# Kernel tuning notes

Measured on AMD Instinct MI355X. Metric: run time of the kernel, lower is better.

## Reference

```python
import jax, jax.numpy as jnp
import numpy as np

N = 40000          # nodes
E = 640000         # edges (avg in-degree ~16)
D_IN = 128         # in_dim == out_dim
E_DIM = 16         # edge feature dim
N_AGG = 6          # mean max min std dir1-av dir1-dx
N_SC = 3           # identity amplification attenuation
AVG_D_LOG = float(np.log(16.0))  # avg_d['log']
EPS = 1e-8
STD_EPS = 1e-5


def setup_inputs() -> dict:
    key = jax.random.key(0)
    ks = jax.random.split(key, 10)
    h = jax.random.normal(ks[0], (N, D_IN), jnp.float32)
    e = jax.random.normal(ks[1], (E, E_DIM), jnp.float32)
    eig = jax.random.normal(ks[2], (N, 2), jnp.float32)
    snorm_n = jax.random.uniform(ks[3], (N, 1), jnp.float32)
    src = jax.random.randint(ks[4], (E,), 0, N)
    dst = jax.random.randint(ks[5], (E,), 0, N)
    pre_in = 2 * D_IN + E_DIM
    W_pre = jax.random.normal(ks[6], (pre_in, D_IN), jnp.float32) / np.sqrt(pre_in)
    b_pre = jnp.zeros((D_IN,), jnp.float32)
    post_in = (N_AGG * N_SC + 1) * D_IN
    W_post = jax.random.normal(ks[7], (post_in, D_IN), jnp.float32) / np.sqrt(post_in)
    b_post = jnp.zeros((D_IN,), jnp.float32)
    return {"h": h, "e": e, "eig": eig, "snorm_n": snorm_n, "src": src,
            "dst": dst, "W_pre": W_pre, "b_pre": b_pre,
            "W_post": W_post, "b_post": b_post}


def reference(h, e, eig, snorm_n, src, dst, W_pre, b_pre, W_post, b_post):
    # --- pretrans on edges: MLP(cat(h_src, h_dst, ef)) -> [E, D_IN]
    z = jnp.concatenate([h[src], h[dst], e], axis=1)
    m = z @ W_pre + b_pre

    seg = lambda x: jax.ops.segment_sum(x, dst, num_segments=N)
    deg = seg(jnp.ones((E,), m.dtype))          # in-degree per node [N]
    has = deg > 0
    degc = jnp.maximum(deg, 1.0)

    # --- mailbox aggregators (edge-parallel segment reductions over dst)
    s1 = seg(m)
    mean = s1 / degc[:, None]
    var = seg(m * m) / degc[:, None] - mean * mean
    std = jnp.sqrt(jnp.maximum(var, 0.0) + STD_EPS)
    mx = jnp.where(has[:, None], jax.ops.segment_max(m, dst, num_segments=N), 0.0)
    mn = jnp.where(has[:, None], jax.ops.segment_min(m, dst, num_segments=N), 0.0)
    # eigenvector-directional aggregators (eig index 1), normalized per dst
    d = eig[src, 1] - eig[dst, 1]                              # [E]
    denom = seg(jnp.abs(d)) + EPS                              # [N]
    dir_av = seg(m * (jnp.abs(d) / denom[dst])[:, None])
    dir_dx = seg(m * (d / denom[dst])[:, None]) - h            # uses h_in

    agg = jnp.concatenate([mean, mx, mn, std, dir_av, dir_dx], axis=1)
    agg = jnp.where(has[:, None], agg, 0.0)  # DGL leaves zeros for isolated nodes

    # --- degree scalers: identity / amplification / attenuation
    logd = jnp.log(degc + 1.0)
    amp = agg * (logd / AVG_D_LOG)[:, None]
    att = agg * (AVG_D_LOG / logd)[:, None]
    hcat = jnp.concatenate([h, agg, amp, att], axis=1)  # [N, 19*D_IN]

    # --- posttrans MLP + graph norm + relu + residual (dropout p=0, no batchnorm)
    out = hcat @ W_post + b_post
    out = out * snorm_n
    out = jax.nn.relu(out)
    out = h + out
    return out
```

## Files before the change

kernel.cpp:

```cpp
#include <hip/hip_runtime.h>
#include <hip/hip_bf16.h>
#include <math.h>

typedef __attribute__((ext_vector_type(4))) float f32x4;
typedef __attribute__((ext_vector_type(2))) float f32x2;
typedef __attribute__((ext_vector_type(8))) short short8;
typedef unsigned short ushort_t;
typedef unsigned int uint_t;

__device__ __forceinline__ float b2f(unsigned short u) {
    unsigned int v = ((unsigned int)u) << 16;
    return __uint_as_float(v);
}
__device__ __forceinline__ unsigned short f2b(float f) {
    unsigned int x = __float_as_uint(f);
    unsigned int r = (x + 0x7fffu + ((x >> 16) & 1u)) >> 16;
    return (unsigned short)r;
}

__global__ void prep_kernel(const float* __restrict__ W_pre,
                            const float* __restrict__ W_post,
                            const float* __restrict__ h,
                            int* __restrict__ counts,
                            ushort_t* __restrict__ WbT,
                            ushort_t* __restrict__ WcT,
                            ushort_t* __restrict__ X, int Nn) {
    int i = blockIdx.x * 256 + threadIdx.x;
    int n0 = Nn + 1;
    if (i < n0) { counts[i] = 0; return; }
    i -= n0;
    if (i < 256 * 128) {
        int nn = i >> 7, k = i & 127;
        float v = (nn < 128) ? W_pre[k * 128 + nn] : W_pre[(128 + k) * 128 + (nn - 128)];
        WbT[i] = f2b(v);
        return;
    }
    i -= 256 * 128;
    if (i < 384 * 896) {
        int nn = i / 896, k = i % 896;
        float v;
        if (k < 128) {
            v = (nn < 128) ? W_post[k * 128 + nn] : 0.f;
        } else {
            int ka = k - 128;
            if (nn < 128)      v = W_post[(128 + ka) * 128 + nn];
            else if (nn < 256) v = W_post[(896 + ka) * 128 + (nn - 128)];
            else               v = W_post[(1664 + ka) * 128 + (nn - 256)];
        }
        WcT[i] = f2b(v);
        return;
    }
    i -= 384 * 896;
    if (i < Nn * 32) {
        int n = i >> 5, c4 = (i & 31) * 4;
        float4 hv = *(const float4*)&h[(size_t)n * 128 + c4];
        ushort4 o;
        o.x = f2b(hv.x); o.y = f2b(hv.y); o.z = f2b(hv.z); o.w = f2b(hv.w);
        *(ushort4*)&X[(size_t)n * 896 + c4] = o;
    }
}

__global__ void hist_kernel(const int* __restrict__ dst, int* __restrict__ counts, int E) {
    int i = blockIdx.x * 256 + threadIdx.x;
    if (i < E) atomicAdd(&counts[dst[i]], 1);
}

__global__ __launch_bounds__(1024) void scan_kernel(int* __restrict__ counts,
                                                    int* __restrict__ cursors, int Nn) {
    __shared__ int part[1024];
    int t = threadIdx.x;
    int base = t * 40;
    int vals[40];
#pragma unroll
    for (int c = 0; c < 10; ++c) {
        int idx = base + c * 4;
        int4 v4 = (idx + 3 < Nn) ? *(const int4*)&counts[idx]
                  : make_int4(idx < Nn ? counts[idx] : 0,
                              idx + 1 < Nn ? counts[idx + 1] : 0,
                              idx + 2 < Nn ? counts[idx + 2] : 0,
                              idx + 3 < Nn ? counts[idx + 3] : 0);
        vals[c * 4] = v4.x; vals[c * 4 + 1] = v4.y;
        vals[c * 4 + 2] = v4.z; vals[c * 4 + 3] = v4.w;
    }
    int loc[40];
    int s = 0;
#pragma unroll
    for (int i = 0; i < 40; ++i) { loc[i] = s; s += vals[i]; }
    part[t] = s;
    __syncthreads();
    for (int off = 1; off < 1024; off <<= 1) {
        int v = part[t];
        int u = (t >= off) ? part[t - off] : 0;
        __syncthreads();
        part[t] = v + u;
        __syncthreads();
    }
    int pre = (t > 0) ? part[t - 1] : 0;
#pragma unroll
    for (int i = 0; i < 40; ++i) {
        int idx = base + i;
        if (idx < Nn) { int o = pre + loc[i]; counts[idx] = o; cursors[idx] = o; }
    }
    if (t == 1023) counts[Nn] = part[1023];
}

__global__ void scatter_kernel(const int* __restrict__ dst, const int* __restrict__ src,
                               const float* __restrict__ eig, int* __restrict__ cursors,
                               int4* __restrict__ esl, int E) {
    int i = blockIdx.x * 256 + threadIdx.x;
    if (i < E) {
        int v = dst[i];
        int p = atomicAdd(&cursors[v], 1);
        int s = src[i];
        esl[p] = make_int4(s, i, __float_as_int(eig[s * 2 + 1]), 0);
    }
}

template <int OUT_BF16>
__global__ __launch_bounds__(256) void gemm_bt(const ushort_t* __restrict__ A, int lda,
                                               const ushort_t* __restrict__ Bt, int ldb,
                                               void* __restrict__ Cv, int ldc,
                                               int M, int K, int NT) {
    __shared__ ushort_t ldsbuf[2 * 128 * 64];
    const int tid = threadIdx.x, wid = tid >> 6, lane = tid & 63;
    int nwg = gridDim.x;
    int orig = blockIdx.x;
    int q8 = nwg >> 3, r8 = nwg & 7;
    int xcd = orig & 7, local = orig >> 3;
    int wg = (xcd < r8 ? xcd * (q8 + 1) : r8 * (q8 + 1) + (xcd - r8) * q8) + local;
    const int m0 = (wg / NT) * 128, n0 = (wg % NT) * 128;
    f32x4 acc[4][4] = {};
    const int wrow = (wid >> 1) * 64, wcol = (wid & 1) * 64;

    for (int kt = 0; kt < K; kt += 64) {
#pragma unroll
        for (int rnd = 0; rnd < 4; ++rnd) {
            int libase = rnd * 256 + wid * 64;
            {
                int lc = libase + lane;
                int r = lc >> 3, cs = lc & 7;
                int c = cs ^ (r & 7);
                int row = m0 + r; row = row < M ? row : M - 1;
                const ushort_t* g = A + (size_t)row * lda + (kt + c * 8);
                __builtin_amdgcn_global_load_lds(
                    (const __attribute__((address_space(1))) unsigned int*)g,
                    (__attribute__((address_space(3))) unsigned int*)&ldsbuf[(size_t)libase * 8],
                    16, 0, 0);
            }
            {
                int lc = libase + lane;
                int r = lc >> 3, cs = lc & 7;
                int c = cs ^ (r & 7);
                const ushort_t* g = Bt + (size_t)(n0 + r) * ldb + (kt + c * 8);
                __builtin_amdgcn_global_load_lds(
                    (const __attribute__((address_space(1))) unsigned int*)g,
                    (__attribute__((address_space(3))) unsigned int*)&ldsbuf[8192 + (size_t)libase * 8],
                    16, 0, 0);
            }
        }
        __syncthreads();
#pragma unroll
        for (int kk = 0; kk < 2; ++kk) {
            short8 af[4], bfr[4];
#pragma unroll
            for (int f = 0; f < 4; ++f) {
                int r = wrow + f * 16 + (lane & 15);
                int c16 = kk * 4 + (lane >> 4);
                int ch = r * 8 + (c16 ^ (r & 7));
                af[f] = *(const short8*)&ldsbuf[ch * 8];
            }
#pragma unroll
            for (int f = 0; f < 4; ++f) {
                int r = wcol + f * 16 + (lane & 15);
                int c16 = kk * 4 + (lane >> 4);
                int ch = r * 8 + (c16 ^ (r & 7));
                bfr[f] = *(const short8*)&ldsbuf[8192 + ch * 8];
            }
#pragma unroll
            for (int i = 0; i < 4; ++i)
#pragma unroll
                for (int j = 0; j < 4; ++j)
                    acc[i][j] = __builtin_amdgcn_mfma_f32_16x16x32_bf16(af[i], bfr[j], acc[i][j], 0, 0, 0);
        }
        __syncthreads();
    }
#pragma unroll
    for (int i = 0; i < 4; ++i)
#pragma unroll
        for (int j = 0; j < 4; ++j)
#pragma unroll
            for (int q = 0; q < 4; ++q) {
                int row = m0 + wrow + i * 16 + (lane >> 4) * 4 + q;
                int col = n0 + wcol + j * 16 + (lane & 15);
                if (row < M) {
                    if (OUT_BF16) ((ushort_t*)Cv)[(size_t)row * ldc + col] = f2b(acc[i][j][q]);
                    else          ((float*)Cv)[(size_t)row * ldc + col] = acc[i][j][q];
                }
            }
}

#define RLI(v, l) __builtin_amdgcn_readlane((v), (l))
__global__ __launch_bounds__(256) void agg_coop(
    const ushort_t* __restrict__ PQ, ushort_t* __restrict__ X,
    const int4* __restrict__ esl, const int* __restrict__ offs,
    const float* __restrict__ eig, const float* __restrict__ h,
    const float* __restrict__ ef, const float* __restrict__ W_pre,
    const float* __restrict__ b_pre, float* __restrict__ scal, int Nn) {
    int tid = threadIdx.x;
    int wid = tid >> 6, lane = tid & 63;
    int n = blockIdx.x * 4 + wid;
    if (n >= Nn) return;
    int off0 = offs[n], off1 = offs[n + 1];
    int deg = off1 - off0;
    int d0 = lane * 2;

    f32x2 w3r[16];
#pragma unroll
    for (int j = 0; j < 16; ++j)
        w3r[j] = *(const f32x2*)&W_pre[(256 + j) * 128 + d0];

    uint_t qw = *(const uint_t*)&PQ[(size_t)n * 256 + 128 + d0];
    float2 bp = *(const float2*)&b_pre[d0];
    f32x2 qb;
    qb.x = b2f((ushort_t)(qw & 0xffff)) + bp.x;
    qb.y = b2f((ushort_t)(qw >> 16)) + bp.y;
    float eigd = eig[n * 2 + 1];

    f32x2 s = {0.f, 0.f}, ss = {0.f, 0.f}, av = {0.f, 0.f}, dv = {0.f, 0.f};
    f32x2 mx = {-1e30f, -1e30f}, mn = {1e30f, 1e30f};
    float den = 0.f;

    for (int q0 = off0; q0 < off1; q0 += 16) {
        int cnt = off1 - q0; if (cnt > 16) cnt = 16;
        int slot = q0 + (lane & 15);
        if (slot > off1 - 1) slot = off1 - 1;
        int4 rc = esl[slot];
        int eidL = __shfl(rc.y, lane >> 2);
        float4 efv = ((const float4*)ef)[(size_t)eidL * 4 + (lane & 3)];
        uint_t pw[16];
#pragma unroll
        for (int j = 0; j < 16; ++j) {
            if (j < cnt) {
                int sj = RLI(rc.x, j);
                pw[j] = *(const uint_t*)&PQ[(size_t)sj * 256 + d0];
            }
        }
#pragma unroll
        for (int j = 0; j < 16; ++j) {
            if (j < cnt) {
                f32x2 acc = qb;
#pragma unroll
                for (int b = 0; b < 4; ++b) {
                    float va = __uint_as_float((uint_t)RLI(__float_as_int(efv.x), 4 * j + b));
                    float vb = __uint_as_float((uint_t)RLI(__float_as_int(efv.y), 4 * j + b));
                    float vc = __uint_as_float((uint_t)RLI(__float_as_int(efv.z), 4 * j + b));
                    float vd = __uint_as_float((uint_t)RLI(__float_as_int(efv.w), 4 * j + b));
                    acc = va * w3r[4 * b + 0] + acc;
                    acc = vb * w3r[4 * b + 1] + acc;
                    acc = vc * w3r[4 * b + 2] + acc;
                    acc = vd * w3r[4 * b + 3] + acc;
                }
                f32x2 m;
                m.x = b2f((ushort_t)(pw[j] & 0xffff));
                m.y = b2f((ushort_t)(pw[j] >> 16));
                m = m + acc;
                float dd = __int_as_float(RLI(rc.z, j)) - eigd;
                float ad = fabsf(dd);
                s = s + m; ss = m * m + ss;
                mx = __builtin_elementwise_max(mx, m);
                mn = __builtin_elementwise_min(mn, m);
                av = ad * m + av; dv = dd * m + dv;
                den += ad;
            }
        }
    }

    size_t xb = (size_t)n * 896 + 128;
    float2 hv = *(const float2*)&h[(size_t)n * 128 + d0];
    float o[12];
    if (deg > 0) {
        float inv = 1.f / (float)deg;
        float mean0 = s.x * inv, mean1 = s.y * inv;
        float var0 = fmaxf(ss.x * inv - mean0 * mean0, 0.f);
        float var1 = fmaxf(ss.y * inv - mean1 * mean1, 0.f);
        float sd0 = sqrtf(var0 + 1e-5f), sd1 = sqrtf(var1 + 1e-5f);
        float idn = 1.f / (den + 1e-8f);
        o[0] = mean0; o[1] = mean1; o[2] = mx.x; o[3] = mx.y; o[4] = mn.x; o[5] = mn.y;
        o[6] = sd0; o[7] = sd1; o[8] = av.x * idn; o[9] = av.y * idn;
        o[10] = dv.x * idn - hv.x; o[11] = dv.y * idn - hv.y;
    } else {
#pragma unroll
        for (int k = 0; k < 12; ++k) o[k] = 0.f;
    }
#pragma unroll
    for (int a = 0; a < 6; ++a) {
        uint_t w = (uint_t)f2b(o[2 * a]) | ((uint_t)f2b(o[2 * a + 1]) << 16);
        *(uint_t*)&X[xb + a * 128 + d0] = w;
    }
    if (lane == 0) {
        float degc = deg > 0 ? (float)deg : 1.f;
        float logd = logf(degc + 1.f);
        scal[n * 2] = logd * (1.f / 2.772588722239781f);
        scal[n * 2 + 1] = 2.772588722239781f / logd;
    }
}

__global__ __launch_bounds__(256) void epilogue_kernel(
    const float* __restrict__ O3, const float* __restrict__ h,
    const float* __restrict__ snorm, const float* __restrict__ scal,
    const float* __restrict__ b_post, float* __restrict__ out, int Nn) {
    int g = blockIdx.x * 256 + threadIdx.x;
    if (g >= Nn * 32) return;
    int n = g >> 5, c4 = (g & 31) * 4;
    float a = scal[n * 2], b = scal[n * 2 + 1], sn = snorm[n];
    const float* base = O3 + (size_t)n * 384 + c4;
    float4 o1 = *(const float4*)base;
    float4 o2 = *(const float4*)(base + 128);
    float4 o3 = *(const float4*)(base + 256);
    float4 bp = *(const float4*)&b_post[c4];
    float4 hv = *(const float4*)&h[(size_t)n * 128 + c4];
    float4 r;
    r.x = fmaxf((o1.x + a * o2.x + b * o3.x + bp.x) * sn, 0.f) + hv.x;
    r.y = fmaxf((o1.y + a * o2.y + b * o3.y + bp.y) * sn, 0.f) + hv.y;
    r.z = fmaxf((o1.z + a * o2.z + b * o3.z + bp.z) * sn, 0.f) + hv.z;
    r.w = fmaxf((o1.w + a * o2.w + b * o3.w + bp.w) * sn, 0.f) + hv.w;
    *(float4*)&out[(size_t)n * 128 + c4] = r;
}

extern "C" void kernel_launch(void* const* d_in, const int* in_sizes, int n_in,
                              void* d_out, int out_size, void* d_ws, size_t ws_size,
                              hipStream_t stream) {
    const float* h      = (const float*)d_in[0];
    const float* ef     = (const float*)d_in[1];
    const float* eig    = (const float*)d_in[2];
    const float* snorm  = (const float*)d_in[3];
    const int*   src    = (const int*)d_in[4];
    const int*   dst    = (const int*)d_in[5];
    const float* W_pre  = (const float*)d_in[6];
    const float* b_pre  = (const float*)d_in[7];
    const float* W_post = (const float*)d_in[8];
    const float* b_post = (const float*)d_in[9];
    int Nn = in_sizes[0] / 128;
    int E  = in_sizes[4];
    float* out = (float*)d_out;

    char* ws = (char*)d_ws;
    size_t off = 0;
    auto alloc = [&](size_t bytes) {
        size_t o = off;
        off = (off + bytes + 255) & ~(size_t)255;
        return o;
    };
    size_t o_counts  = alloc(((size_t)Nn + 1) * 4);
    size_t o_cursors = alloc((size_t)Nn * 4);
    size_t o_esl     = alloc((size_t)E * 16);
    size_t o_PQ      = alloc((size_t)Nn * 256 * 2);
    size_t o_X       = alloc((size_t)Nn * 896 * 2);
    size_t o_O3      = alloc((size_t)Nn * 384 * 4);
    size_t o_scal    = alloc((size_t)Nn * 2 * 4);
    size_t o_wb      = alloc(256 * 128 * 2);
    size_t o_wc      = alloc(384 * 896 * 2);
    (void)ws_size;

    int*      counts  = (int*)(ws + o_counts);
    int*      cursors = (int*)(ws + o_cursors);
    int4*     esl     = (int4*)(ws + o_esl);
    ushort_t* PQ      = (ushort_t*)(ws + o_PQ);
    ushort_t* X       = (ushort_t*)(ws + o_X);
    float*    O3      = (float*)(ws + o_O3);
    float*    scal    = (float*)(ws + o_scal);
    ushort_t* WbT     = (ushort_t*)(ws + o_wb);
    ushort_t* WcT     = (ushort_t*)(ws + o_wc);

    int prep_items = (Nn + 1) + 256 * 128 + 384 * 896 + Nn * 32;
    prep_kernel<<<(prep_items + 255) / 256, 256, 0, stream>>>(W_pre, W_post, h,
                                                              counts, WbT, WcT, X, Nn);
    hist_kernel<<<(E + 255) / 256, 256, 0, stream>>>(dst, counts, E);
    scan_kernel<<<1, 1024, 0, stream>>>(counts, cursors, Nn);
    scatter_kernel<<<(E + 255) / 256, 256, 0, stream>>>(dst, src, eig, cursors, esl, E);

    int mt = (Nn + 127) / 128;
    gemm_bt<1><<<mt * 2, 256, 0, stream>>>(X, 896, WbT, 128, (void*)PQ, 256, Nn, 128, 2);

    agg_coop<<<(Nn + 3) / 4, 256, 0, stream>>>(PQ, X, esl, counts, eig, h, ef,
                                               W_pre, b_pre, scal, Nn);

    gemm_bt<0><<<mt * 3, 256, 0, stream>>>(X, 896, WcT, 896, (void*)O3, 384, Nn, 896, 3);

    epilogue_kernel<<<(Nn * 32 + 255) / 256, 256, 0, stream>>>(O3, h, snorm, scal, b_post,
                                                               out, Nn);
}
```

Measured before the change: 271.5 us.

## Materialize scaled aggregates in full-width X and fuse epilogue into single post GEMM

Instead of running a 896-wide K GEMM that produces three 128-column partial outputs (identity, amp, att) and recombining them in a separate epilogue, the aggregation kernel now writes the amp- and att-scaled aggregates directly into a 2432-wide bf16 row. A new 64-row-tile MFMA GEMM with K=2432 and N=128 then applies bias, snorm, relu and the residual in its epilogue. This removes the fp32 O3 intermediate, the scal buffer and the epilogue launch. In exchange it writes about 2.7x more bf16 activation data per node, adds an extra rounding of the scaled aggregates, and the GEMM K loop is not double-buffered.

```diff
diff --git a/kernel.cpp b/kernel.cpp
--- a/kernel.cpp
+++ b/kernel.cpp
@@ -17,6 +17,11 @@
     unsigned int r = (x + 0x7fffu + ((x >> 16) & 1u)) >> 16;
     return (unsigned short)r;
 }
+__device__ __forceinline__ uint_t pack2(float a, float b) {
+    return (uint_t)f2b(a) | ((uint_t)f2b(b) << 16);
+}
+
+#define XW 2432
 
 __global__ void prep_kernel(const float* __restrict__ W_pre,
                             const float* __restrict__ W_post,
@@ -36,27 +41,18 @@
         return;
     }
     i -= 256 * 128;
-    if (i < 384 * 896) {
-        int nn = i / 896, k = i % 896;
-        float v;
-        if (k < 128) {
-            v = (nn < 128) ? W_post[k * 128 + nn] : 0.f;
-        } else {
-            int ka = k - 128;
-            if (nn < 128)      v = W_post[(128 + ka) * 128 + nn];
-            else if (nn < 256) v = W_post[(896 + ka) * 128 + (nn - 128)];
-            else               v = W_post[(1664 + ka) * 128 + (nn - 256)];
-        }
-        WcT[i] = f2b(v);
+    if (i < 128 * XW) {
+        int nn = i / XW, k = i % XW;
+        WcT[i] = f2b(W_post[(size_t)k * 128 + nn]);
         return;
     }
-    i -= 384 * 896;
+    i -= 128 * XW;
     if (i < Nn * 32) {
         int n = i >> 5, c4 = (i & 31) * 4;
         float4 hv = *(const float4*)&h[(size_t)n * 128 + c4];
         ushort4 o;
         o.x = f2b(hv.x); o.y = f2b(hv.y); o.z = f2b(hv.z); o.w = f2b(hv.w);
-        *(ushort4*)&X[(size_t)n * 896 + c4] = o;
+        *(ushort4*)&X[(size_t)n * XW + c4] = o;
     }
 }
 
@@ -199,13 +195,93 @@
             }
 }
 
+__global__ __launch_bounds__(256) void gemm_final(
+    const ushort_t* __restrict__ A, const ushort_t* __restrict__ Bt,
+    const float* __restrict__ h, const float* __restrict__ snorm,
+    const float* __restrict__ b_post, float* __restrict__ out, int M) {
+    __shared__ ushort_t ldsA[64 * 64];
+    __shared__ ushort_t ldsB[128 * 64];
+    const int tid = threadIdx.x, wid = tid >> 6, lane = tid & 63;
+    int nwg = gridDim.x, orig = blockIdx.x;
+    int q8 = nwg >> 3, r8 = nwg & 7;
+    int xcd = orig & 7, local = orig >> 3;
+    int wg = (xcd < r8 ? xcd * (q8 + 1) : r8 * (q8 + 1) + (xcd - r8) * q8) + local;
+    const int m0 = wg * 64;
+    f32x4 acc[2][4] = {};
+    const int wrow = (wid >> 1) * 32, wcol = (wid & 1) * 64;
+
+    for (int kt = 0; kt < XW; kt += 64) {
+#pragma unroll
+        for (int rnd = 0; rnd < 2; ++rnd) {
+            int lc = rnd * 256 + tid;
+            int r = lc >> 3, cs = lc & 7;
+            int c = cs ^ (r & 7);
+            int row = m0 + r; row = row < M ? row : M - 1;
+            const ushort_t* g = A + (size_t)row * XW + (kt + c * 8);
+            __builtin_amdgcn_global_load_lds(
+                (const __attribute__((address_space(1))) unsigned int*)g,
+                (__attribute__((address_space(3))) unsigned int*)&ldsA[(size_t)lc * 8],
+                16, 0, 0);
+        }
+#pragma unroll
+        for (int rnd = 0; rnd < 4; ++rnd) {
+            int lc = rnd * 256 + tid;
+            int r = lc >> 3, cs = lc & 7;
+            int c = cs ^ (r & 7);
+            const ushort_t* g = Bt + (size_t)r * XW + (kt + c * 8);
+            __builtin_amdgcn_global_load_lds(
+                (const __attribute__((address_space(1))) unsigned int*)g,
+                (__attribute__((address_space(3))) unsigned int*)&ldsB[(size_t)lc * 8],
+                16, 0, 0);
+        }
+        __syncthreads();
+#pragma unroll
+        for (int kk = 0; kk < 2; ++kk) {
+            int c16 = kk * 4 + (lane >> 4);
+            short8 af[2], bfr[4];
+#pragma unroll
+            for (int f = 0; f < 2; ++f) {
+                int r = wrow + f * 16 + (lane & 15);
+                af[f] = *(const short8*)&ldsA[(r * 8 + (c16 ^ (r & 7))) * 8];
+            }
+#pragma unroll
+            for (int f = 0; f < 4; ++f) {
+                int r = wcol + f * 16 + (lane & 15);
+                bfr[f] = *(const short8*)&ldsB[(r * 8 + (c16 ^ (r & 7))) * 8];
+            }
+#pragma unroll
+            for (int i = 0; i < 2; ++i)
+#pragma unroll
+                for (int j = 0; j < 4; ++j)
+                    acc[i][j] = __builtin_amdgcn_mfma_f32_16x16x32_bf16(af[i], bfr[j], acc[i][j], 0, 0, 0);
+        }
+        __syncthreads();
+    }
+#pragma unroll
+    for (int i = 0; i < 2; ++i)
+#pragma unroll
+        for (int q = 0; q < 4; ++q) {
+            int row = m0 + wrow + i * 16 + (lane >> 4) * 4 + q;
+            if (row < M) {
+                float sn = snorm[row];
+#pragma unroll
+                for (int j = 0; j < 4; ++j) {
+                    int col = wcol + j * 16 + (lane & 15);
+                    float v = (acc[i][j][q] + b_post[col]) * sn;
+                    out[(size_t)row * 128 + col] =
+                        fmaxf(v, 0.f) + h[(size_t)row * 128 + col];
+                }
+            }
+        }
+}
+
 #define RLI(v, l) __builtin_amdgcn_readlane((v), (l))
 __global__ __launch_bounds__(256) void agg_coop(
     const ushort_t* __restrict__ PQ, ushort_t* __restrict__ X,
     const int4* __restrict__ esl, const int* __restrict__ offs,
     const float* __restrict__ eig, const float* __restrict__ h,
     const float* __restrict__ ef, const float* __restrict__ W_pre,
-    const float* __restrict__ b_pre, float* __restrict__ scal, int Nn) {
+    const float* __restrict__ b_pre, int Nn) {
     int tid = threadIdx.x;
     int wid = tid >> 6, lane = tid & 63;
     int n = blockIdx.x * 4 + wid;
@@ -275,7 +351,7 @@
         }
     }
 
-    size_t xb = (size_t)n * 896 + 128;
+    size_t xb = (size_t)n * XW + 128;
     float2 hv = *(const float2*)&h[(size_t)n * 128 + d0];
     float o[12];
     if (deg > 0) {
@@ -292,39 +368,17 @@
 #pragma unroll
         for (int k = 0; k < 12; ++k) o[k] = 0.f;
     }
+    float degc = deg > 0 ? (float)deg : 1.f;
+    float logd = logf(degc + 1.f);
+    float amp = logd * (1.f / 2.772588722239781f);
+    float att = 2.772588722239781f / logd;
 #pragma unroll
     for (int a = 0; a < 6; ++a) {
-        uint_t w = (uint_t)f2b(o[2 * a]) | ((uint_t)f2b(o[2 * a + 1]) << 16);
-        *(uint_t*)&X[xb + a * 128 + d0] = w;
-    }
-    if (lane == 0) {
-        float degc = deg > 0 ? (float)deg : 1.f;
-        float logd = logf(degc + 1.f);
-        scal[n * 2] = logd * (1.f / 2.772588722239781f);
-        scal[n * 2 + 1] = 2.772588722239781f / logd;
-    }
-}
-
-__global__ __launch_bounds__(256) void epilogue_kernel(
-    const float* __restrict__ O3, const float* __restrict__ h,
-    const float* __restrict__ snorm, const float* __restrict__ scal,
-    const float* __restrict__ b_post, float* __restrict__ out, int Nn) {
-    int g = blockIdx.x * 256 + threadIdx.x;
-    if (g >= Nn * 32) return;
-    int n = g >> 5, c4 = (g & 31) * 4;
-    float a = scal[n * 2], b = scal[n * 2 + 1], sn = snorm[n];
-    const float* base = O3 + (size_t)n * 384 + c4;
-    float4 o1 = *(const float4*)base;
-    float4 o2 = *(const float4*)(base + 128);
-    float4 o3 = *(const float4*)(base + 256);
-    float4 bp = *(const float4*)&b_post[c4];
-    float4 hv = *(const float4*)&h[(size_t)n * 128 + c4];
-    float4 r;
-    r.x = fmaxf((o1.x + a * o2.x + b * o3.x + bp.x) * sn, 0.f) + hv.x;
-    r.y = fmaxf((o1.y + a * o2.y + b * o3.y + bp.y) * sn, 0.f) + hv.y;
-    r.z = fmaxf((o1.z + a * o2.z + b * o3.z + bp.z) * sn, 0.f) + hv.z;
-    r.w = fmaxf((o1.w + a * o2.w + b * o3.w + bp.w) * sn, 0.f) + hv.w;
-    *(float4*)&out[(size_t)n * 128 + c4] = r;
+        float o0 = o[2 * a], o1 = o[2 * a + 1];
+        *(uint_t*)&X[xb + a * 128 + d0]        = pack2(o0, o1);
+        *(uint_t*)&X[xb + 768 + a * 128 + d0]  = pack2(o0 * amp, o1 * amp);
+        *(uint_t*)&X[xb + 1536 + a * 128 + d0] = pack2(o0 * att, o1 * att);
+    }
 }
 
 extern "C" void kernel_launch(void* const* d_in, const int* in_sizes, int n_in,
@@ -355,11 +409,9 @@
     size_t o_cursors = alloc((size_t)Nn * 4);
     size_t o_esl     = alloc((size_t)E * 16);
     size_t o_PQ      = alloc((size_t)Nn * 256 * 2);
-    size_t o_X       = alloc((size_t)Nn * 896 * 2);
-    size_t o_O3      = alloc((size_t)Nn * 384 * 4);
-    size_t o_scal    = alloc((size_t)Nn * 2 * 4);
+    size_t o_X       = alloc((size_t)Nn * XW * 2);
     size_t o_wb      = alloc(256 * 128 * 2);
-    size_t o_wc      = alloc(384 * 896 * 2);
+    size_t o_wc      = alloc(128 * XW * 2);
     (void)ws_size;
 
     int*      counts  = (int*)(ws + o_counts);
@@ -367,12 +419,10 @@
     int4*     esl     = (int4*)(ws + o_esl);
     ushort_t* PQ      = (ushort_t*)(ws + o_PQ);
     ushort_t* X       = (ushort_t*)(ws + o_X);
-    float*    O3      = (float*)(ws + o_O3);
-    float*    scal    = (float*)(ws + o_scal);
     ushort_t* WbT     = (ushort_t*)(ws + o_wb);
     ushort_t* WcT     = (ushort_t*)(ws + o_wc);
 
-    int prep_items = (Nn + 1) + 256 * 128 + 384 * 896 + Nn * 32;
+    int prep_items = (Nn + 1) + 256 * 128 + 128 * XW + Nn * 32;
     prep_kernel<<<(prep_items + 255) / 256, 256, 0, stream>>>(W_pre, W_post, h,
                                                               counts, WbT, WcT, X, Nn);
     hist_kernel<<<(E + 255) / 256, 256, 0, stream>>>(dst, counts, E);
@@ -380,13 +430,11 @@
     scatter_kernel<<<(E + 255) / 256, 256, 0, stream>>>(dst, src, eig, cursors, esl, E);
 
     int mt = (Nn + 127) / 128;
-    gemm_bt<1><<<mt * 2, 256, 0, stream>>>(X, 896, WbT, 128, (void*)PQ, 256, Nn, 128, 2);
+    gemm_bt<1><<<mt * 2, 256, 0, stream>>>(X, XW, WbT, 128, (void*)PQ, 256, Nn, 128, 2);
 
     agg_coop<<<(Nn + 3) / 4, 256, 0, stream>>>(PQ, X, esl, counts, eig, h, ef,
-                                               W_pre, b_pre, scal, Nn);
-
-    gemm_bt<0><<<mt * 3, 256, 0, stream>>>(X, 896, WcT, 896, (void*)O3, 384, Nn, 896, 3);
-
-    epilogue_kernel<<<(Nn * 32 + 255) / 256, 256, 0, stream>>>(O3, h, snorm, scal, b_post,
-                                                               out, Nn);
-}
+                                               W_pre, b_pre, Nn);
+
+    int mt64 = (Nn + 63) / 64;
+    gemm_final<<<mt64, 256, 0, stream>>>(X, WcT, h, snorm, b_post, out, Nn);
+}
```

Result: slower. 299.9 us (+10.5%).

## Parallelize prefix scan across blocks and store post-GEMM output in bf16

Applied to the files above, without the earlier changes.

The single-block 1024-thread scan over node degrees is replaced by a three-phase multi-block scan: per-block local scans, a 64-thread scan of the block sums, then a fixup pass. This removes a serial single-workgroup stage from the CSR build. Separately, the second GEMM now writes its intermediate output in bf16 instead of fp32, halving that buffer's write and read traffic in the epilogue at some cost in precision. The scan assumes at most 64 blocks (Nn up to 65536).

```diff
diff --git a/kernel.cpp b/kernel.cpp
--- a/kernel.cpp
+++ b/kernel.cpp
@@ -65,43 +65,67 @@
     if (i < E) atomicAdd(&counts[dst[i]], 1);
 }
 
-__global__ __launch_bounds__(1024) void scan_kernel(int* __restrict__ counts,
-                                                    int* __restrict__ cursors, int Nn) {
-    __shared__ int part[1024];
+__global__ __launch_bounds__(256) void scanA_kernel(const int* __restrict__ counts,
+                                                    int* __restrict__ localscan,
+                                                    int* __restrict__ blocksum, int Nn) {
+    __shared__ int part[256];
+    int b = blockIdx.x, t = threadIdx.x;
+    int idx = b * 1024 + t * 4;
+    int4 v = (idx + 3 < Nn) ? *(const int4*)&counts[idx]
+             : make_int4(idx < Nn ? counts[idx] : 0,
+                         idx + 1 < Nn ? counts[idx + 1] : 0,
+                         idx + 2 < Nn ? counts[idx + 2] : 0,
+                         idx + 3 < Nn ? counts[idx + 3] : 0);
+    int s1 = v.x, s2 = v.x + v.y, s3 = s2 + v.z, tot = s3 + v.w;
+    part[t] = tot;
+    __syncthreads();
+    for (int off = 1; off < 256; off <<= 1) {
+        int x = part[t];
+        int u = (t >= off) ? part[t - off] : 0;
+        __syncthreads();
+        part[t] = x + u;
+        __syncthreads();
+    }
+    int pre = (t > 0) ? part[t - 1] : 0;
+    if (idx < Nn) {
+        if (idx + 3 < Nn) {
+            *(int4*)&localscan[idx] = make_int4(pre, pre + s1, pre + s2, pre + s3);
+        } else {
+            localscan[idx] = pre;
+            if (idx + 1 < Nn) localscan[idx + 1] = pre + s1;
+            if (idx + 2 < Nn) localscan[idx + 2] = pre + s2;
+        }
+    }
+    if (t == 255) blocksum[b] = part[255];
+}
+
+__global__ __launch_bounds__(64) void scanB_kernel(int* __restrict__ blocksum, int nb) {
+    __shared__ int sh[64];
     int t = threadIdx.x;
-    int base = t * 40;
-    int vals[40];
-#pragma unroll
-    for (int c = 0; c < 10; ++c) {
-        int idx = base + c * 4;
-        int4 v4 = (idx + 3 < Nn) ? *(const int4*)&counts[idx]
-                  : make_int4(idx < Nn ? counts[idx] : 0,
-                              idx + 1 < Nn ? counts[idx + 1] : 0,
-                              idx + 2 < Nn ? counts[idx + 2] : 0,
-                              idx + 3 < Nn ? counts[idx + 3] : 0);
-        vals[c * 4] = v4.x; vals[c * 4 + 1] = v4.y;
-        vals[c * 4 + 2] = v4.z; vals[c * 4 + 3] = v4.w;
-    }
-    int loc[40];
-    int s = 0;
-#pragma unroll
-    for (int i = 0; i < 40; ++i) { loc[i] = s; s += vals[i]; }
-    part[t] = s;
+    int v = (t < nb) ? blocksum[t] : 0;
+    sh[t] = v;
     __syncthreads();
-    for (int off = 1; off < 1024; off <<= 1) {
-        int v = part[t];
-        int u = (t >= off) ? part[t - off] : 0;
-        __syncthreads();
-        part[t] = v + u;
-        __syncthreads();
-    }
-    int pre = (t > 0) ? part[t - 1] : 0;
-#pragma unroll
-    for (int i = 0; i < 40; ++i) {
-        int idx = base + i;
-        if (idx < Nn) { int o = pre + loc[i]; counts[idx] = o; cursors[idx] = o; }
-    }
-    if (t == 1023) counts[Nn] = part[1023];
+    for (int off = 1; off < 64; off <<= 1) {
+        int x = sh[t];
+        int u = (t >= off) ? sh[t - off] : 0;
+        __syncthreads();
+        sh[t] = x + u;
+        __syncthreads();
+    }
+    int pre = (t > 0) ? sh[t - 1] : 0;
+    if (t < nb) blocksum[t] = pre;
+    if (t == 63) blocksum[nb] = sh[63];
+}
+
+__global__ void scanC_kernel(int* __restrict__ localscan, const int* __restrict__ blocksum,
+                             int* __restrict__ counts, int Nn, int nb) {
+    int i = blockIdx.x * 256 + threadIdx.x;
+    if (i < Nn) {
+        int o = localscan[i] + blocksum[blockIdx.x >> 2];
+        counts[i] = o;
+        localscan[i] = o;
+    }
+    if (i == 0) counts[Nn] = blocksum[nb];
 }
 
 __global__ void scatter_kernel(const int* __restrict__ dst, const int* __restrict__ src,
@@ -306,24 +330,24 @@
 }
 
 __global__ __launch_bounds__(256) void epilogue_kernel(
-    const float* __restrict__ O3, const float* __restrict__ h,
+    const ushort_t* __restrict__ O3, const float* __restrict__ h,
     const float* __restrict__ snorm, const float* __restrict__ scal,
     const float* __restrict__ b_post, float* __restrict__ out, int Nn) {
     int g = blockIdx.x * 256 + threadIdx.x;
     if (g >= Nn * 32) return;
     int n = g >> 5, c4 = (g & 31) * 4;
     float a = scal[n * 2], b = scal[n * 2 + 1], sn = snorm[n];
-    const float* base = O3 + (size_t)n * 384 + c4;
-    float4 o1 = *(const float4*)base;
-    float4 o2 = *(const float4*)(base + 128);
-    float4 o3 = *(const float4*)(base + 256);
+    const ushort_t* base = O3 + (size_t)n * 384 + c4;
+    ushort4 u1 = *(const ushort4*)base;
+    ushort4 u2 = *(const ushort4*)(base + 128);
+    ushort4 u3 = *(const ushort4*)(base + 256);
     float4 bp = *(const float4*)&b_post[c4];
     float4 hv = *(const float4*)&h[(size_t)n * 128 + c4];
     float4 r;
-    r.x = fmaxf((o1.x + a * o2.x + b * o3.x + bp.x) * sn, 0.f) + hv.x;
-    r.y = fmaxf((o1.y + a * o2.y + b * o3.y + bp.y) * sn, 0.f) + hv.y;
-    r.z = fmaxf((o1.z + a * o2.z + b * o3.z + bp.z) * sn, 0.f) + hv.z;
-    r.w = fmaxf((o1.w + a * o2.w + b * o3.w + bp.w) * sn, 0.f) + hv.w;
+    r.x = fmaxf((b2f(u1.x) + a * b2f(u2.x) + b * b2f(u3.x) + bp.x) * sn, 0.f) + hv.x;
+    r.y = fmaxf((b2f(u1.y) + a * b2f(u2.y) + b * b2f(u3.y) + bp.y) * sn, 0.f) + hv.y;
+    r.z = fmaxf((b2f(u1.z) + a * b2f(u2.z) + b * b2f(u3.z) + bp.z) * sn, 0.f) + hv.z;
+    r.w = fmaxf((b2f(u1.w) + a * b2f(u2.w) + b * b2f(u3.w) + bp.w) * sn, 0.f) + hv.w;
     *(float4*)&out[(size_t)n * 128 + c4] = r;
 }
 
@@ -353,10 +377,11 @@
     };
     size_t o_counts  = alloc(((size_t)Nn + 1) * 4);
     size_t o_cursors = alloc((size_t)Nn * 4);
+    size_t o_bsum    = alloc(65 * 4);
     size_t o_esl     = alloc((size_t)E * 16);
     size_t o_PQ      = alloc((size_t)Nn * 256 * 2);
     size_t o_X       = alloc((size_t)Nn * 896 * 2);
-    size_t o_O3      = alloc((size_t)Nn * 384 * 4);
+    size_t o_O3      = alloc((size_t)Nn * 384 * 2);
     size_t o_scal    = alloc((size_t)Nn * 2 * 4);
     size_t o_wb      = alloc(256 * 128 * 2);
     size_t o_wc      = alloc(384 * 896 * 2);
@@ -364,10 +389,11 @@
 
     int*      counts  = (int*)(ws + o_counts);
     int*      cursors = (int*)(ws + o_cursors);
+    int*      bsum    = (int*)(ws + o_bsum);
     int4*     esl     = (int4*)(ws + o_esl);
     ushort_t* PQ      = (ushort_t*)(ws + o_PQ);
     ushort_t* X       = (ushort_t*)(ws + o_X);
-    float*    O3      = (float*)(ws + o_O3);
+    ushort_t* O3      = (ushort_t*)(ws + o_O3);
     float*    scal    = (float*)(ws + o_scal);
     ushort_t* WbT     = (ushort_t*)(ws + o_wb);
     ushort_t* WcT     = (ushort_t*)(ws + o_wc);
@@ -376,7 +402,10 @@
     prep_kernel<<<(prep_items + 255) / 256, 256, 0, stream>>>(W_pre, W_post, h,
                                                               counts, WbT, WcT, X, Nn);
     hist_kernel<<<(E + 255) / 256, 256, 0, stream>>>(dst, counts, E);
-    scan_kernel<<<1, 1024, 0, stream>>>(counts, cursors, Nn);
+    int nb = (Nn + 1023) / 1024;
+    scanA_kernel<<<nb, 256, 0, stream>>>(counts, cursors, bsum, Nn);
+    scanB_kernel<<<1, 64, 0, stream>>>(bsum, nb);
+    scanC_kernel<<<(Nn + 255) / 256, 256, 0, stream>>>(cursors, bsum, counts, Nn, nb);
     scatter_kernel<<<(E + 255) / 256, 256, 0, stream>>>(dst, src, eig, cursors, esl, E);
 
     int mt = (Nn + 127) / 128;
@@ -385,7 +414,7 @@
     agg_coop<<<(Nn + 3) / 4, 256, 0, stream>>>(PQ, X, esl, counts, eig, h, ef,
                                                W_pre, b_pre, scal, Nn);
 
-    gemm_bt<0><<<mt * 3, 256, 0, stream>>>(X, 896, WcT, 896, (void*)O3, 384, Nn, 896, 3);
+    gemm_bt<1><<<mt * 3, 256, 0, stream>>>(X, 896, WcT, 896, (void*)O3, 384, Nn, 896, 3);
 
     epilogue_kernel<<<(Nn * 32 + 255) / 256, 256, 0, stream>>>(O3, h, snorm, scal, b_post,
                                                                out, Nn);
```

Measured after the change: 226.8 us, median of 2. 1.2x faster.
